# Optimization experiments

Hardware: AMD Instinct MI355X
Metric: run time of the kernel (lower is better)

## Reference

```python
import jax, jax.numpy as jnp
import numpy as np

N_NODES = 100000
N_EDGES = 1600000
IN_DIM = 128
HID_DIM = 64
OUT_DIM = 128
EPS = 1e-5


def setup_inputs() -> dict:
    key = jax.random.key(0)
    ks = jax.random.split(key, 10)
    feat = jax.random.normal(ks[0], (N_NODES, IN_DIM), dtype=jnp.float32)
    src = jax.random.randint(ks[1], (N_EDGES,), 0, N_NODES)
    dst = jax.random.randint(ks[2], (N_EDGES,), 0, N_NODES)
    # learned params
    gamma = jnp.ones((IN_DIM,), jnp.float32)
    beta = jnp.zeros((IN_DIM,), jnp.float32)
    Wq = jax.random.normal(ks[3], (IN_DIM, HID_DIM), jnp.float32) * 0.05
    bq = jax.random.normal(ks[4], (HID_DIM,), jnp.float32) * 0.05
    Wk = jax.random.normal(ks[5], (IN_DIM, HID_DIM), jnp.float32) * 0.05
    Wv = jax.random.normal(ks[6], (IN_DIM, OUT_DIM), jnp.float32) * 0.05
    We = jax.random.normal(ks[7], (HID_DIM, 1), jnp.float32) * 0.05
    return {"feat": feat, "src": src, "dst": dst, "gamma": gamma, "beta": beta,
            "Wq": Wq, "bq": bq, "Wk": Wk, "Wv": Wv, "We": We}


def reference(feat, src, dst, gamma, beta, Wq, bq, Wk, Wv, We):
    # BatchNorm1d (training-mode batch stats, biased variance)
    mean = jnp.mean(feat, axis=0)
    var = jnp.mean((feat - mean) ** 2, axis=0)
    x = (feat - mean) * jax.lax.rsqrt(var + EPS) * gamma + beta
    # feat_drop = 0.0 -> identity
    q = x @ Wq + bq          # [N, H]
    k = x @ Wk               # [N, H]
    v = x @ Wv               # [N, O]
    # u_add_v: src-node q + dst-node k per edge, then sigmoid and fc_e -> scalar score
    e = jax.nn.sigmoid(q[src] + k[dst]) @ We  # [E, 1]
    e = e[:, 0]                               # [E]
    # edge_softmax: softmax over incoming edges of each destination node
    m = jax.ops.segment_max(e, dst, num_segments=N_NODES)  # [N]
    ex = jnp.exp(e - m[dst])
    s = jax.ops.segment_sum(ex, dst, num_segments=N_NODES)  # [N]
    a = ex / s[dst]                                          # [E]
    # u_mul_e_sum: weighted scatter-sum of source v into destinations
    rst = jax.ops.segment_sum(v[src] * a[:, None], dst, num_segments=N_NODES)  # [N, O]
    return rst
```

## Files before the change

kernel.cpp:

```cpp
#include <hip/hip_runtime.h>
#include <math.h>

#define IN_DIM 128
#define HID 64
#define OUT_DIM 128
#define ELL_W 64
#define NWG 64
#define SCAN_B 256
constexpr float EPS = 1e-5f;

typedef short short8 __attribute__((ext_vector_type(8)));
typedef float f32x4  __attribute__((ext_vector_type(4)));


__device__ inline ushort f2bf(float x) {
    __bf16 h = (__bf16)x;
    return *reinterpret_cast<ushort*>(&h);
}
__device__ inline short f2bfs(float x) {
    __bf16 h = (__bf16)x;
    return *reinterpret_cast<short*>(&h);
}
__device__ inline float bf2f(ushort u) {
    union { unsigned u; float f; } c; c.u = ((unsigned)u) << 16;
    return c.f;
}
__device__ inline float4 bf4_to_f4(ushort4 u) {
    return make_float4(bf2f(u.x), bf2f(u.y), bf2f(u.z), bf2f(u.w));
}

__global__ __launch_bounds__(256) void stats_kernel(
    const float* __restrict__ feat, float* __restrict__ ws, int n_nodes)
{
    int col  = threadIdx.x & 127;
    int half = threadIdx.x >> 7;
    float sum = 0.f, sq = 0.f;
    for (int r = blockIdx.x * 2 + half; r < n_nodes; r += gridDim.x * 2) {
        float x = feat[r * IN_DIM + col];
        sum += x; sq += x * x;
    }
    __shared__ float redS[256], redQ[256];
    redS[threadIdx.x] = sum; redQ[threadIdx.x] = sq;
    __syncthreads();
    if (threadIdx.x < 128) {
        sum = redS[threadIdx.x] + redS[threadIdx.x + 128];
        sq  = redQ[threadIdx.x] + redQ[threadIdx.x + 128];
        unsafeAtomicAdd(&ws[col], sum);
        unsafeAtomicAdd(&ws[128 + col], sq);
    }
}

__global__ __launch_bounds__(256) void wprep(
    const float* __restrict__ Wq, const float* __restrict__ Wk,
    const float* __restrict__ Wv, ushort* __restrict__ Bfrag)
{
    int gid  = blockIdx.x * 256 + threadIdx.x;
    int f    = gid >> 6;
    int lane = gid & 63;
    int kc = f & 3, ct = (f >> 2) & 3, w = f >> 4;
    int col   = w * 64 + ct * 16 + (lane & 15);
    int kbase = kc * 32 + (lane >> 4) * 8;
    ushort tmp[8];
    #pragma unroll
    for (int j = 0; j < 8; j++) {
        int k = kbase + j;
        float val;
        if (col < 64)       val = Wq[k * HID + col];
        else if (col < 128) val = Wk[k * HID + (col - 64)];
        else                val = Wv[k * OUT_DIM + (col - 128)];
        tmp[j] = f2bf(val);
    }
    ushort* d = &Bfrag[(f * 64 + lane) * 8];
    *(ushort4*)d       = make_ushort4(tmp[0], tmp[1], tmp[2], tmp[3]);
    *(ushort4*)(d + 4) = make_ushort4(tmp[4], tmp[5], tmp[6], tmp[7]);
}

__global__ __launch_bounds__(256) void mfma_qkv(
    const float* __restrict__ feat, const ushort* __restrict__ Bfrag,
    const float* __restrict__ bq,
    const float* __restrict__ gamma, const float* __restrict__ beta,
    const float* __restrict__ stats,
    ushort* __restrict__ qvb, ushort* __restrict__ kb,
    int n_nodes)
{
    __shared__ float sc[IN_DIM], sh[IN_DIM];
    int tid = threadIdx.x;
    if (tid < 128) {
        float inv_n = 1.0f / (float)n_nodes;
        float mean = stats[tid] * inv_n;
        float var  = stats[128 + tid] * inv_n - mean * mean;
        float s    = gamma[tid] * rsqrtf(var + EPS);
        sc[tid] = s; sh[tid] = beta[tid] - mean * s;
    }

    int w    = tid >> 6;
    int lane = tid & 63;
    int row0 = blockIdx.x * 64;
    int m    = lane & 15;
    int quad = lane >> 4;
    int nm1  = n_nodes - 1;

    short8 bfr[16];
    #pragma unroll
    for (int f = 0; f < 16; f++)
        bfr[f] = *(const short8*)&Bfrag[((w * 16 + f) * 64 + lane) * 8];

    __syncthreads();

    f32x4 acc[4][4] = {};

    #pragma unroll
    for (int kc = 0; kc < 4; kc++) {
        int koff = kc * 32 + quad * 8;
        float4 sc0 = *(const float4*)&sc[koff];
        float4 sc1 = *(const float4*)&sc[koff + 4];
        float4 sh0 = *(const float4*)&sh[koff];
        float4 sh1 = *(const float4*)&sh[koff + 4];
        short8 afr[4];
        #pragma unroll
        for (int rt = 0; rt < 4; rt++) {
            int row = row0 + rt * 16 + m;
            row = row < nm1 ? row : nm1;
            const float* fp = &feat[(size_t)row * IN_DIM + koff];
            float4 x0 = *(const float4*)fp;
            float4 x1 = *(const float4*)(fp + 4);
            afr[rt][0] = f2bfs(x0.x * sc0.x + sh0.x);
            afr[rt][1] = f2bfs(x0.y * sc0.y + sh0.y);
            afr[rt][2] = f2bfs(x0.z * sc0.z + sh0.z);
            afr[rt][3] = f2bfs(x0.w * sc0.w + sh0.w);
            afr[rt][4] = f2bfs(x1.x * sc1.x + sh1.x);
            afr[rt][5] = f2bfs(x1.y * sc1.y + sh1.y);
            afr[rt][6] = f2bfs(x1.z * sc1.z + sh1.z);
            afr[rt][7] = f2bfs(x1.w * sc1.w + sh1.w);
        }
        #pragma unroll
        for (int rt = 0; rt < 4; rt++)
            #pragma unroll
            for (int ct = 0; ct < 4; ct++)
                acc[rt][ct] = __builtin_amdgcn_mfma_f32_16x16x32_bf16(
                    afr[rt], bfr[ct * 4 + kc], acc[rt][ct], 0, 0, 0);
    }

    ushort* base; int ld, cl;
    if (w == 1)      { base = kb;  ld = HID; cl = 0; }
    else             { base = qvb; ld = 192; cl = (w == 0) ? 0 : 64 * (w - 1); }

    #pragma unroll
    for (int ct = 0; ct < 4; ct++) {
        int col = cl + ct * 16 + m;
        float bias = (w == 0) ? bq[ct * 16 + m] : 0.f;
        #pragma unroll
        for (int rt = 0; rt < 4; rt++) {
            int r0 = row0 + rt * 16 + quad * 4;
            #pragma unroll
            for (int r = 0; r < 4; r++)
                base[(size_t)(r0 + r) * ld + col] = f2bf(acc[rt][ct][r] + bias);
        }
    }
}

__global__ __launch_bounds__(256) void hist_bins(
    const int* __restrict__ dst, int* __restrict__ histT,
    int n_edges, int nbk, int chunk)
{
    extern __shared__ int cnt[];
    int w = blockIdx.x, t = threadIdx.x;
    for (int b = t; b < nbk; b += 256) cnt[b] = 0;
    __syncthreads();
    int lo = w * chunk;
    int hi = lo + chunk; if (hi > n_edges) hi = n_edges;
    for (int e = lo + t; e < hi; e += 256)
        atomicAdd(&cnt[dst[e] >> 6], 1);
    __syncthreads();
    for (int b = t; b < nbk; b += 256)
        histT[b * NWG + w] = cnt[b];
}

__global__ __launch_bounds__(256) void scan_partial(
    const int* __restrict__ deg, int* __restrict__ part, int n)
{
    int chunk = (n + SCAN_B - 1) / SCAN_B;
    int lo = blockIdx.x * chunk;
    int hi = lo + chunk; if (hi > n) hi = n;
    int s = 0;
    for (int i = lo + threadIdx.x; i < hi; i += 256) s += deg[i];
    __shared__ int red[256];
    red[threadIdx.x] = s; __syncthreads();
    for (int d = 128; d; d >>= 1) {
        if (threadIdx.x < d) red[threadIdx.x] += red[threadIdx.x + d];
        __syncthreads();
    }
    if (threadIdx.x == 0) part[blockIdx.x] = red[0];
}

__global__ __launch_bounds__(256) void scan_combine(
    int* __restrict__ part, int* __restrict__ offsets, int n)
{
    __shared__ int tmp[256];
    int t = threadIdx.x;
    int v = part[t];
    tmp[t] = v; __syncthreads();
    for (int d = 1; d < 256; d <<= 1) {
        int cur = tmp[t];
        int add = (t >= d) ? tmp[t - d] : 0;
        __syncthreads();
        tmp[t] = cur + add;
        __syncthreads();
    }
    part[t] = tmp[t] - v;
    if (t == 255) offsets[n] = tmp[255];
}

__global__ __launch_bounds__(256) void scan_final(
    const int* __restrict__ deg, const int* __restrict__ part,
    int* __restrict__ offsets, int* __restrict__ cursor, int n)
{
    __shared__ int tmp[256];
    int t = threadIdx.x;
    int chunk = (n + SCAN_B - 1) / SCAN_B;
    int lo = blockIdx.x * chunk;
    int hi = lo + chunk; if (hi > n) hi = n;
    int base = part[blockIdx.x];
    for (int i0 = lo; i0 < hi; i0 += 256) {
        int i = i0 + t;
        int d = (i < hi) ? deg[i] : 0;
        tmp[t] = d; __syncthreads();
        for (int s = 1; s < 256; s <<= 1) {
            int cur = tmp[t];
            int add = (t >= s) ? tmp[t - s] : 0;
            __syncthreads();
            tmp[t] = cur + add;
            __syncthreads();
        }
        int excl = tmp[t] - d;
        int total = tmp[255];
        if (i < hi) { offsets[i] = base + excl; cursor[i] = base + excl; }
        base += total;
        __syncthreads();
    }
}

__global__ __launch_bounds__(256) void scatter_bins(
    const int* __restrict__ src, const int* __restrict__ dst,
    const int* __restrict__ offs, int* __restrict__ packed,
    int n_edges, int nbk, int chunk)
{
    extern __shared__ int cur[];
    int w = blockIdx.x, t = threadIdx.x;
    for (int b = t; b < nbk; b += 256) cur[b] = offs[b * NWG + w];
    __syncthreads();
    int lo = w * chunk;
    int hi = lo + chunk; if (hi > n_edges) hi = n_edges;
    for (int e = lo + t; e < hi; e += 256) {
        int d = dst[e];
        int b = d >> 6;
        int pos = atomicAdd(&cur[b], 1);
        packed[pos] = (int)(((unsigned)(d & 63) << 26) | (unsigned)src[e]);
    }
}

__device__ __forceinline__ void gather_core(
    const int* row, int cnt, int node, int h, int sub,
    const ushort* __restrict__ qvb, const ushort* __restrict__ kb,
    const float* __restrict__ We, float* __restrict__ out)
{
    if (cnt == 0) {
        if (sub == 0) {
            float4 z = make_float4(0.f, 0.f, 0.f, 0.f);
            *(float4*)&out[node * OUT_DIM + 4 * h]      = z;
            *(float4*)&out[node * OUT_DIM + 64 + 4 * h] = z;
        }
        return;
    }

    float4 kd = bf4_to_f4(*(const ushort4*)&kb[node * HID + 4 * h]);
    float4 we = *(const float4*)&We[4 * h];

    float4 o0 = make_float4(0.f, 0.f, 0.f, 0.f);
    float4 o1 = make_float4(0.f, 0.f, 0.f, 0.f);
    float ssum = 0.f;

    for (int p0 = 0; p0 < cnt; p0 += 4) {
        int p = p0 + sub;
        bool act = (p < cnt);
        int sN = row[act ? p : 0];
        const ushort* qv = qvb + (size_t)sN * 192;
        float4 qq = bf4_to_f4(*(const ushort4*)(qv + 4 * h));
        float t;
        t  = we.x * __fdividef(1.f, 1.f + __expf(-(qq.x + kd.x)));
        t += we.y * __fdividef(1.f, 1.f + __expf(-(qq.y + kd.y)));
        t += we.z * __fdividef(1.f, 1.f + __expf(-(qq.z + kd.z)));
        t += we.w * __fdividef(1.f, 1.f + __expf(-(qq.w + kd.w)));
        t += __shfl_xor(t, 1);
        t += __shfl_xor(t, 2);
        t += __shfl_xor(t, 4);
        t += __shfl_xor(t, 8);
        float exv = act ? __expf(t) : 0.f;
        ssum += exv;
        float4 v0 = bf4_to_f4(*(const ushort4*)(qv + 64 + 4 * h));
        float4 v1 = bf4_to_f4(*(const ushort4*)(qv + 128 + 4 * h));
        o0.x += exv * v0.x; o0.y += exv * v0.y;
        o0.z += exv * v0.z; o0.w += exv * v0.w;
        o1.x += exv * v1.x; o1.y += exv * v1.y;
        o1.z += exv * v1.z; o1.w += exv * v1.w;
    }

    ssum += __shfl_xor(ssum, 16); ssum += __shfl_xor(ssum, 32);
    o0.x += __shfl_xor(o0.x, 16); o0.x += __shfl_xor(o0.x, 32);
    o0.y += __shfl_xor(o0.y, 16); o0.y += __shfl_xor(o0.y, 32);
    o0.z += __shfl_xor(o0.z, 16); o0.z += __shfl_xor(o0.z, 32);
    o0.w += __shfl_xor(o0.w, 16); o0.w += __shfl_xor(o0.w, 32);
    o1.x += __shfl_xor(o1.x, 16); o1.x += __shfl_xor(o1.x, 32);
    o1.y += __shfl_xor(o1.y, 16); o1.y += __shfl_xor(o1.y, 32);
    o1.z += __shfl_xor(o1.z, 16); o1.z += __shfl_xor(o1.z, 32);
    o1.w += __shfl_xor(o1.w, 16); o1.w += __shfl_xor(o1.w, 32);

    if (sub == 0) {
        float inv = (ssum > 0.f) ? __fdividef(1.f, ssum) : 0.f;
        o0.x *= inv; o0.y *= inv; o0.z *= inv; o0.w *= inv;
        o1.x *= inv; o1.y *= inv; o1.z *= inv; o1.w *= inv;
        *(float4*)&out[node * OUT_DIM + 4 * h]      = o0;
        *(float4*)&out[node * OUT_DIM + 64 + 4 * h] = o1;
    }
}

__global__ __launch_bounds__(256) void gather_fused(
    const int* __restrict__ offs, const int* __restrict__ packed,
    const ushort* __restrict__ qvb, const ushort* __restrict__ kb,
    const float* __restrict__ We,
    float* __restrict__ out, int n_nodes)
{
    __shared__ int deg_l[64];
    __shared__ int ell_l[64][ELL_W];
    int b = blockIdx.x;
    int t = threadIdx.x;
    if (t < 64) deg_l[t] = 0;
    __syncthreads();

    int beg = offs[b * NWG];
    int end = offs[(b + 1) * NWG];
    for (int e = beg + t; e < end; e += 256) {
        int p = packed[e];
        int dl = (int)((unsigned)p >> 26);
        int pos = atomicAdd(&deg_l[dl], 1);
        if (pos < ELL_W) ell_l[dl][pos] = p & 0x03FFFFFF;
    }
    __syncthreads();

    int wv   = t >> 6;
    int lane = t & 63;
    int h    = lane & 15;
    int sub  = lane >> 4;
    #pragma unroll 1
    for (int i = 0; i < 16; i++) {
        int dl = wv * 16 + i;
        int node = (b << 6) + dl;
        if (node >= n_nodes) break;
        int cnt = deg_l[dl];
        cnt = cnt < ELL_W ? cnt : ELL_W;
        gather_core(&ell_l[dl][0], cnt, node, h, sub, qvb, kb, We, out);
    }
}

extern "C" void kernel_launch(void* const* d_in, const int* in_sizes, int n_in,
                              void* d_out, int out_size, void* d_ws, size_t ws_size,
                              hipStream_t stream)
{
    const float* feat  = (const float*)d_in[0];
    const int*   src   = (const int*)d_in[1];
    const int*   dst   = (const int*)d_in[2];
    const float* gamma = (const float*)d_in[3];
    const float* beta  = (const float*)d_in[4];
    const float* Wq    = (const float*)d_in[5];
    const float* bq    = (const float*)d_in[6];
    const float* Wk    = (const float*)d_in[7];
    const float* Wv    = (const float*)d_in[8];
    const float* We    = (const float*)d_in[9];

    int n_nodes = in_sizes[0] / IN_DIM;
    int n_edges = in_sizes[1];
    int n_pad   = n_nodes + 64;
    int nbk     = (n_nodes + 63) >> 6;
    int nidx    = nbk * NWG;
    int chunk   = (n_edges + NWG - 1) / NWG;

    float* ws = (float*)d_ws;

    int* histT  = (int*)(ws + 256);
    int* offs   = histT + nidx;
    int* part   = offs + nidx + 1;
    int* cursor = part + SCAN_B;
    int* packed = cursor + nidx + 1;
    size_t off = 256 + (size_t)(nidx) + (nidx + 1) + SCAN_B + (nidx + 1)
               + (size_t)n_edges;
    off = (off + 3) & ~(size_t)3;
    ushort* qvb   = (ushort*)(ws + off);
    ushort* kb    = qvb + (size_t)n_pad * 192;
    ushort* Bfrag = kb + (size_t)n_pad * HID;

    size_t lds_bins = (size_t)nbk * sizeof(int);

    hipMemsetAsync(ws, 0, 256 * sizeof(float), stream);
    stats_kernel<<<256, 256, 0, stream>>>(feat, ws, n_nodes);
    wprep<<<16, 256, 0, stream>>>(Wq, Wk, Wv, Bfrag);
    hist_bins<<<NWG, 256, lds_bins, stream>>>(dst, histT, n_edges, nbk, chunk);
    scan_partial<<<SCAN_B, 256, 0, stream>>>(histT, part, nidx);
    scan_combine<<<1, 256, 0, stream>>>(part, offs, nidx);
    scan_final<<<SCAN_B, 256, 0, stream>>>(histT, part, offs, cursor, nidx);
    scatter_bins<<<NWG, 256, lds_bins, stream>>>(
        src, dst, offs, packed, n_edges, nbk, chunk);
    mfma_qkv<<<(n_nodes + 63) / 64, 256, 0, stream>>>(
        feat, Bfrag, bq, gamma, beta, ws, qvb, kb, n_nodes);
    gather_fused<<<nbk, 256, 0, stream>>>(
        offs, packed, qvb, kb, We, (float*)d_out, n_nodes);
}
```

Before: 488.9 us.

## Fuse preprocessing kernels and replace per-workgroup histogram scan with bucket-level atomics

Merges the stats, histogram and weight-prep kernels into one launch split by block range. The per-(bucket, workgroup) histogram and three-stage scan become global per-bucket counts, a single-block scan, and a scatter that reserves bucket ranges with global atomics. It also halves the bucket size to 32 nodes so the gather runs twice as many blocks. The aim is fewer launches and a much smaller scan, at the cost of a serial single-block scan over about 3125 buckets, a second pass over dst inside scatter, and a nondeterministic edge order within each bucket.

Result: faster. 429.7 us (-12.1%).

```diff
diff --git a/kernel.cpp b/kernel.cpp
--- a/kernel.cpp
+++ b/kernel.cpp
@@ -5,8 +5,8 @@
 #define HID 64
 #define OUT_DIM 128
 #define ELL_W 64
-#define NWG 64
-#define SCAN_B 256
+#define BKT 32
+#define HWG 64
 constexpr float EPS = 1e-5f;
 
 typedef short short8 __attribute__((ext_vector_type(8)));
@@ -29,50 +29,123 @@
     return make_float4(bf2f(u.x), bf2f(u.y), bf2f(u.z), bf2f(u.w));
 }
 
-__global__ __launch_bounds__(256) void stats_kernel(
-    const float* __restrict__ feat, float* __restrict__ ws, int n_nodes)
-{
-    int col  = threadIdx.x & 127;
-    int half = threadIdx.x >> 7;
-    float sum = 0.f, sq = 0.f;
-    for (int r = blockIdx.x * 2 + half; r < n_nodes; r += gridDim.x * 2) {
-        float x = feat[r * IN_DIM + col];
-        sum += x; sq += x * x;
-    }
-    __shared__ float redS[256], redQ[256];
-    redS[threadIdx.x] = sum; redQ[threadIdx.x] = sq;
-    __syncthreads();
-    if (threadIdx.x < 128) {
-        sum = redS[threadIdx.x] + redS[threadIdx.x + 128];
-        sq  = redQ[threadIdx.x] + redQ[threadIdx.x + 128];
-        unsafeAtomicAdd(&ws[col], sum);
-        unsafeAtomicAdd(&ws[128 + col], sq);
-    }
-}
-
-__global__ __launch_bounds__(256) void wprep(
+__global__ __launch_bounds__(256) void pre_kernel(
+    const float* __restrict__ feat, float* __restrict__ ws, int n_nodes,
+    const int* __restrict__ dst, int* __restrict__ bcnt, int n_edges,
     const float* __restrict__ Wq, const float* __restrict__ Wk,
-    const float* __restrict__ Wv, ushort* __restrict__ Bfrag)
-{
-    int gid  = blockIdx.x * 256 + threadIdx.x;
-    int f    = gid >> 6;
-    int lane = gid & 63;
-    int kc = f & 3, ct = (f >> 2) & 3, w = f >> 4;
-    int col   = w * 64 + ct * 16 + (lane & 15);
-    int kbase = kc * 32 + (lane >> 4) * 8;
-    ushort tmp[8];
-    #pragma unroll
-    for (int j = 0; j < 8; j++) {
-        int k = kbase + j;
-        float val;
-        if (col < 64)       val = Wq[k * HID + col];
-        else if (col < 128) val = Wk[k * HID + (col - 64)];
-        else                val = Wv[k * OUT_DIM + (col - 128)];
-        tmp[j] = f2bf(val);
-    }
-    ushort* d = &Bfrag[(f * 64 + lane) * 8];
-    *(ushort4*)d       = make_ushort4(tmp[0], tmp[1], tmp[2], tmp[3]);
-    *(ushort4*)(d + 4) = make_ushort4(tmp[4], tmp[5], tmp[6], tmp[7]);
+    const float* __restrict__ Wv, ushort* __restrict__ Bfrag,
+    int nbk, int chunk)
+{
+    extern __shared__ int sm[];
+    int t = threadIdx.x;
+
+    if (blockIdx.x < 256) {
+        float* redS = (float*)sm;
+        float* redQ = redS + 256;
+        int col  = t & 127;
+        int half = t >> 7;
+        float sum = 0.f, sq = 0.f;
+        for (int r = blockIdx.x * 2 + half; r < n_nodes; r += 512) {
+            float x = feat[r * IN_DIM + col];
+            sum += x; sq += x * x;
+        }
+        redS[t] = sum; redQ[t] = sq;
+        __syncthreads();
+        if (t < 128) {
+            sum = redS[t] + redS[t + 128];
+            sq  = redQ[t] + redQ[t + 128];
+            unsafeAtomicAdd(&ws[col], sum);
+            unsafeAtomicAdd(&ws[128 + col], sq);
+        }
+    } else if (blockIdx.x < 256 + HWG) {
+        int w = blockIdx.x - 256;
+        for (int b = t; b < nbk; b += 256) sm[b] = 0;
+        __syncthreads();
+        int lo = w * chunk;
+        int hi = lo + chunk; if (hi > n_edges) hi = n_edges;
+        for (int e = lo + t; e < hi; e += 256)
+            atomicAdd(&sm[__builtin_nontemporal_load(dst + e) >> 5], 1);
+        __syncthreads();
+        for (int b = t; b < nbk; b += 256)
+            if (sm[b]) atomicAdd(&bcnt[b], sm[b]);
+    } else {
+        int gid  = (blockIdx.x - 256 - HWG) * 256 + t;
+        int f    = gid >> 6;
+        int lane = gid & 63;
+        int kc = f & 3, ct = (f >> 2) & 3, w = f >> 4;
+        int col   = w * 64 + ct * 16 + (lane & 15);
+        int kbase = kc * 32 + (lane >> 4) * 8;
+        ushort tmp[8];
+        #pragma unroll
+        for (int j = 0; j < 8; j++) {
+            int k = kbase + j;
+            float val;
+            if (col < 64)       val = Wq[k * HID + col];
+            else if (col < 128) val = Wk[k * HID + (col - 64)];
+            else                val = Wv[k * OUT_DIM + (col - 128)];
+            tmp[j] = f2bf(val);
+        }
+        ushort* d = &Bfrag[(f * 64 + lane) * 8];
+        *(ushort4*)d       = make_ushort4(tmp[0], tmp[1], tmp[2], tmp[3]);
+        *(ushort4*)(d + 4) = make_ushort4(tmp[4], tmp[5], tmp[6], tmp[7]);
+    }
+}
+
+__global__ __launch_bounds__(256) void scan_init(
+    const int* __restrict__ bcnt, int* __restrict__ offs,
+    int* __restrict__ cursor, int n)
+{
+    __shared__ int tmp[256];
+    int t = threadIdx.x;
+    int base = 0;
+    for (int i0 = 0; i0 < n; i0 += 256) {
+        int i = i0 + t;
+        int d = (i < n) ? bcnt[i] : 0;
+        tmp[t] = d; __syncthreads();
+        for (int s = 1; s < 256; s <<= 1) {
+            int cur = tmp[t];
+            int add = (t >= s) ? tmp[t - s] : 0;
+            __syncthreads();
+            tmp[t] = cur + add;
+            __syncthreads();
+        }
+        int excl = tmp[t] - d;
+        if (i < n) { offs[i] = base + excl; cursor[i] = base + excl; }
+        base += tmp[255];
+        __syncthreads();
+    }
+    if (t == 0) offs[n] = base;
+}
+
+__global__ __launch_bounds__(512) void scatter_bins(
+    const int* __restrict__ src, const int* __restrict__ dst,
+    int* __restrict__ cursor, int* __restrict__ packed,
+    int n_edges, int nbk, int chunk)
+{
+    extern __shared__ int sm[];
+    int* cnt  = sm;
+    int* base = sm + nbk;
+    int w = blockIdx.x, t = threadIdx.x;
+    for (int b = t; b < nbk; b += 512) cnt[b] = 0;
+    __syncthreads();
+    int lo = w * chunk;
+    int hi = lo + chunk; if (hi > n_edges) hi = n_edges;
+    for (int e = lo + t; e < hi; e += 512)
+        atomicAdd(&cnt[__builtin_nontemporal_load(dst + e) >> 5], 1);
+    __syncthreads();
+    for (int b = t; b < nbk; b += 512) {
+        int c = cnt[b];
+        if (c) base[b] = atomicAdd(&cursor[b], c);
+        cnt[b] = 0;
+    }
+    __syncthreads();
+    for (int e = lo + t; e < hi; e += 512) {
+        int d = __builtin_nontemporal_load(dst + e);
+        int s = __builtin_nontemporal_load(src + e);
+        int b = d >> 5;
+        int pos = base[b] + atomicAdd(&cnt[b], 1);
+        packed[pos] = (int)(((unsigned)(d & 31) << 26) | (unsigned)s);
+    }
 }
 
 __global__ __launch_bounds__(256) void mfma_qkv(
@@ -159,106 +232,6 @@
     }
 }
 
-__global__ __launch_bounds__(256) void hist_bins(
-    const int* __restrict__ dst, int* __restrict__ histT,
-    int n_edges, int nbk, int chunk)
-{
-    extern __shared__ int cnt[];
-    int w = blockIdx.x, t = threadIdx.x;
-    for (int b = t; b < nbk; b += 256) cnt[b] = 0;
-    __syncthreads();
-    int lo = w * chunk;
-    int hi = lo + chunk; if (hi > n_edges) hi = n_edges;
-    for (int e = lo + t; e < hi; e += 256)
-        atomicAdd(&cnt[dst[e] >> 6], 1);
-    __syncthreads();
-    for (int b = t; b < nbk; b += 256)
-        histT[b * NWG + w] = cnt[b];
-}
-
-__global__ __launch_bounds__(256) void scan_partial(
-    const int* __restrict__ deg, int* __restrict__ part, int n)
-{
-    int chunk = (n + SCAN_B - 1) / SCAN_B;
-    int lo = blockIdx.x * chunk;
-    int hi = lo + chunk; if (hi > n) hi = n;
-    int s = 0;
-    for (int i = lo + threadIdx.x; i < hi; i += 256) s += deg[i];
-    __shared__ int red[256];
-    red[threadIdx.x] = s; __syncthreads();
-    for (int d = 128; d; d >>= 1) {
-        if (threadIdx.x < d) red[threadIdx.x] += red[threadIdx.x + d];
-        __syncthreads();
-    }
-    if (threadIdx.x == 0) part[blockIdx.x] = red[0];
-}
-
-__global__ __launch_bounds__(256) void scan_combine(
-    int* __restrict__ part, int* __restrict__ offsets, int n)
-{
-    __shared__ int tmp[256];
-    int t = threadIdx.x;
-    int v = part[t];
-    tmp[t] = v; __syncthreads();
-    for (int d = 1; d < 256; d <<= 1) {
-        int cur = tmp[t];
-        int add = (t >= d) ? tmp[t - d] : 0;
-        __syncthreads();
-        tmp[t] = cur + add;
-        __syncthreads();
-    }
-    part[t] = tmp[t] - v;
-    if (t == 255) offsets[n] = tmp[255];
-}
-
-__global__ __launch_bounds__(256) void scan_final(
-    const int* __restrict__ deg, const int* __restrict__ part,
-    int* __restrict__ offsets, int* __restrict__ cursor, int n)
-{
-    __shared__ int tmp[256];
-    int t = threadIdx.x;
-    int chunk = (n + SCAN_B - 1) / SCAN_B;
-    int lo = blockIdx.x * chunk;
-    int hi = lo + chunk; if (hi > n) hi = n;
-    int base = part[blockIdx.x];
-    for (int i0 = lo; i0 < hi; i0 += 256) {
-        int i = i0 + t;
-        int d = (i < hi) ? deg[i] : 0;
-        tmp[t] = d; __syncthreads();
-        for (int s = 1; s < 256; s <<= 1) {
-            int cur = tmp[t];
-            int add = (t >= s) ? tmp[t - s] : 0;
-            __syncthreads();
-            tmp[t] = cur + add;
-            __syncthreads();
-        }
-        int excl = tmp[t] - d;
-        int total = tmp[255];
-        if (i < hi) { offsets[i] = base + excl; cursor[i] = base + excl; }
-        base += total;
-        __syncthreads();
-    }
-}
-
-__global__ __launch_bounds__(256) void scatter_bins(
-    const int* __restrict__ src, const int* __restrict__ dst,
-    const int* __restrict__ offs, int* __restrict__ packed,
-    int n_edges, int nbk, int chunk)
-{
-    extern __shared__ int cur[];
-    int w = blockIdx.x, t = threadIdx.x;
-    for (int b = t; b < nbk; b += 256) cur[b] = offs[b * NWG + w];
-    __syncthreads();
-    int lo = w * chunk;
-    int hi = lo + chunk; if (hi > n_edges) hi = n_edges;
-    for (int e = lo + t; e < hi; e += 256) {
-        int d = dst[e];
-        int b = d >> 6;
-        int pos = atomicAdd(&cur[b], 1);
-        packed[pos] = (int)(((unsigned)(d & 63) << 26) | (unsigned)src[e]);
-    }
-}
-
 __device__ __forceinline__ void gather_core(
     const int* row, int cnt, int node, int h, int sub,
     const ushort* __restrict__ qvb, const ushort* __restrict__ kb,
@@ -330,15 +303,15 @@
     const float* __restrict__ We,
     float* __restrict__ out, int n_nodes)
 {
-    __shared__ int deg_l[64];
-    __shared__ int ell_l[64][ELL_W];
+    __shared__ int deg_l[BKT];
+    __shared__ int ell_l[BKT][ELL_W];
     int b = blockIdx.x;
     int t = threadIdx.x;
-    if (t < 64) deg_l[t] = 0;
-    __syncthreads();
-
-    int beg = offs[b * NWG];
-    int end = offs[(b + 1) * NWG];
+    if (t < BKT) deg_l[t] = 0;
+    __syncthreads();
+
+    int beg = offs[b];
+    int end = offs[b + 1];
     for (int e = beg + t; e < end; e += 256) {
         int p = packed[e];
         int dl = (int)((unsigned)p >> 26);
@@ -352,9 +325,9 @@
     int h    = lane & 15;
     int sub  = lane >> 4;
     #pragma unroll 1
-    for (int i = 0; i < 16; i++) {
-        int dl = wv * 16 + i;
-        int node = (b << 6) + dl;
+    for (int i = 0; i < BKT / 4; i++) {
+        int dl = wv * (BKT / 4) + i;
+        int node = b * BKT + dl;
         if (node >= n_nodes) break;
         int cnt = deg_l[dl];
         cnt = cnt < ELL_W ? cnt : ELL_W;
@@ -380,35 +353,30 @@
     int n_nodes = in_sizes[0] / IN_DIM;
     int n_edges = in_sizes[1];
     int n_pad   = n_nodes + 64;
-    int nbk     = (n_nodes + 63) >> 6;
-    int nidx    = nbk * NWG;
-    int chunk   = (n_edges + NWG - 1) / NWG;
+    int nbk     = (n_nodes + BKT - 1) / BKT;
+    int chunk   = (n_edges + HWG - 1) / HWG;
 
     float* ws = (float*)d_ws;
 
-    int* histT  = (int*)(ws + 256);
-    int* offs   = histT + nidx;
-    int* part   = offs + nidx + 1;
-    int* cursor = part + SCAN_B;
-    int* packed = cursor + nidx + 1;
-    size_t off = 256 + (size_t)(nidx) + (nidx + 1) + SCAN_B + (nidx + 1)
-               + (size_t)n_edges;
+    int* bcnt   = (int*)(ws + 256);
+    int* offs   = bcnt + nbk;
+    int* cursor = offs + nbk + 1;
+    int* packed = cursor + nbk;
+    size_t off = 256 + (size_t)nbk + (nbk + 1) + nbk + (size_t)n_edges;
     off = (off + 3) & ~(size_t)3;
     ushort* qvb   = (ushort*)(ws + off);
     ushort* kb    = qvb + (size_t)n_pad * 192;
     ushort* Bfrag = kb + (size_t)n_pad * HID;
 
-    size_t lds_bins = (size_t)nbk * sizeof(int);
-
-    hipMemsetAsync(ws, 0, 256 * sizeof(float), stream);
-    stats_kernel<<<256, 256, 0, stream>>>(feat, ws, n_nodes);
-    wprep<<<16, 256, 0, stream>>>(Wq, Wk, Wv, Bfrag);
-    hist_bins<<<NWG, 256, lds_bins, stream>>>(dst, histT, n_edges, nbk, chunk);
-    scan_partial<<<SCAN_B, 256, 0, stream>>>(histT, part, nidx);
-    scan_combine<<<1, 256, 0, stream>>>(part, offs, nidx);
-    scan_final<<<SCAN_B, 256, 0, stream>>>(histT, part, offs, cursor, nidx);
-    scatter_bins<<<NWG, 256, lds_bins, stream>>>(
-        src, dst, offs, packed, n_edges, nbk, chunk);
+    size_t lds_pre  = (size_t)(nbk > 512 ? nbk : 512) * sizeof(int);
+    size_t lds_scat = 2 * (size_t)nbk * sizeof(int);
+
+    hipMemsetAsync(ws, 0, (256 + (size_t)nbk) * sizeof(float), stream);
+    pre_kernel<<<256 + HWG + 16, 256, lds_pre, stream>>>(
+        feat, ws, n_nodes, dst, bcnt, n_edges, Wq, Wk, Wv, Bfrag, nbk, chunk);
+    scan_init<<<1, 256, 0, stream>>>(bcnt, offs, cursor, nbk);
+    scatter_bins<<<HWG, 512, lds_scat, stream>>>(
+        src, dst, cursor, packed, n_edges, nbk, chunk);
     mfma_qkv<<<(n_nodes + 63) / 64, 256, 0, stream>>>(
         feat, Bfrag, bq, gamma, beta, ws, qvb, kb, n_nodes);
     gather_fused<<<nbk, 256, 0, stream>>>(
```
